# Optimization experiments

Measured on AMD Instinct MI355X. Metric: run time of the kernel, lower is better.

## Reference

```python
import jax, jax.numpy as jnp
import numpy as np


def setup_inputs() -> dict:
    key = jax.random.key(0)
    k1, k2 = jax.random.split(key)
    B, S, D = 8, 4096, 1024
    E, P = 8, 4
    x = jax.random.normal(k1, (B, S, D), dtype=jnp.float32)
    phi_kernel = jax.random.normal(k2, (D, E * P), dtype=jnp.float32) * (1.0 / np.sqrt(D))
    phi_bias = jnp.zeros((E * P,), dtype=jnp.float32)
    return {"x": x, "phi_kernel": phi_kernel, "phi_bias": phi_bias,
            "num_experts": E, "num_slots": P}


def reference(x, phi_kernel, phi_bias, num_experts, num_slots):
    B, S, D = x.shape
    E, P = num_experts, num_slots
    # phi logits: [B,S,E,P]
    phi_logits = (jnp.einsum('bsd,dk->bsk', x, phi_kernel) + phi_bias).reshape(B, S, E, P)
    # softmax over the sequence axis (each slot is a convex combo of tokens)
    phi_weights = jax.nn.softmax(phi_logits, axis=1)
    # soft slots: weighted sum over tokens -> [B,E,P,D] (fused, no [B,S,E,P,D] blowup)
    soft_slots = jnp.einsum('bsd,bsep->bepd', x, phi_weights)
    expert_inputs = soft_slots.reshape(B, E, P * D)
    expert_weights = jnp.full((B, S, E), 1.0 / E, dtype=x.dtype)
    expert_indices = jnp.broadcast_to(jnp.arange(E, dtype=jnp.int32)[None, None, :], (B, S, E))
    return (expert_weights, expert_indices, phi_weights, soft_slots, expert_inputs)
```

## Files before the change

### kernel.cpp

```cpp
#include <hip/hip_runtime.h>
#include <hip/hip_bf16.h>

#define B 8
#define S 4096
#define DD 1024
#define KK 32

__global__ __launch_bounds__(256) void k1_logits(const float* __restrict__ x,
                                                 const float* __restrict__ phi,
                                                 const float* __restrict__ bias,
                                                 float* __restrict__ lp) {
    constexpr int DCH = 512, NCH = 16;
    __shared__ float xt[2][64 * 36];

    const int bid = blockIdx.x;
    const int dq  = bid & 1;
    const int st  = (bid >> 1) & 63;
    const int b   = bid >> 7;
    const int s0  = st * 64;
    const int tid = threadIdx.x;
    const int kg  = __builtin_amdgcn_readfirstlane(tid >> 6);
    const int lane = tid & 63;

    float acc[8];
#pragma unroll
    for (int j = 0; j < 8; ++j) acc[j] = (dq == 0) ? bias[kg * 8 + j] : 0.f;

    const float* xb = x + ((size_t)(b * S + s0)) * DD + dq * DCH;
    const int row = tid >> 3;
    const int c4  = tid & 7;

    {
        float4 p0 = *(const float4*)(xb + (size_t)row * DD + c4 * 4);
        float4 p1 = *(const float4*)(xb + (size_t)(row + 32) * DD + c4 * 4);
        *(float4*)(&xt[0][row * 36 + c4 * 4]) = p0;
        *(float4*)(&xt[0][(row + 32) * 36 + c4 * 4]) = p1;
    }
    __syncthreads();

    for (int ch = 0; ch < NCH; ++ch) {
        const int cur = ch & 1;
        float4 q0, q1;
        if (ch + 1 < NCH) {
            q0 = *(const float4*)(xb + (size_t)row * DD + (ch + 1) * 32 + c4 * 4);
            q1 = *(const float4*)(xb + (size_t)(row + 32) * DD + (ch + 1) * 32 + c4 * 4);
        }

        const float* pbase = phi + (size_t)(dq * DCH + ch * 32) * KK + kg * 8;
        const float* xrow  = &xt[cur][lane * 36];
#pragma unroll
        for (int g = 0; g < 8; ++g) {
            float4 a = *(const float4*)(xrow + g * 4);
            const float* ap = &a.x;
#pragma unroll
            for (int dd = 0; dd < 4; ++dd) {
                const float* pr = pbase + (size_t)(g * 4 + dd) * KK;
                float4 pA = *(const float4*)pr;
                float4 pB = *(const float4*)(pr + 4);
                float av = ap[dd];
                acc[0] += av * pA.x; acc[1] += av * pA.y;
                acc[2] += av * pA.z; acc[3] += av * pA.w;
                acc[4] += av * pB.x; acc[5] += av * pB.y;
                acc[6] += av * pB.z; acc[7] += av * pB.w;
            }
        }
        __syncthreads();
        if (ch + 1 < NCH) {
            *(float4*)(&xt[cur ^ 1][row * 36 + c4 * 4]) = q0;
            *(float4*)(&xt[cur ^ 1][(row + 32) * 36 + c4 * 4]) = q1;
        }
        __syncthreads();
    }

    float* o = lp + (((size_t)dq * B + b) * KK + kg * 8) * S + s0;
#pragma unroll
    for (int j = 0; j < 8; ++j) o[(size_t)j * S + lane] = acc[j];
}

__global__ __launch_bounds__(256) void k2a_partial(const float* __restrict__ lp,
                                                   float* __restrict__ pmax,
                                                   float* __restrict__ psum) {
    const int bid = blockIdx.x;
    const int c  = bid & 7;
    const int bk = bid >> 3;
    const int tid = threadIdx.x;
    const int wave = tid >> 6, lane = tid & 63;
    const size_t base = (size_t)bk * S + c * 512;

    float v0 = lp[base + tid]       + lp[1048576 + base + tid];
    float v1 = lp[base + tid + 256] + lp[1048576 + base + tid + 256];

    float m = fmaxf(v0, v1);
#pragma unroll
    for (int off = 32; off >= 1; off >>= 1) m = fmaxf(m, __shfl_xor(m, off, 64));
    __shared__ float sm[4], sl[4];
    if (lane == 0) sm[wave] = m;
    __syncthreads();
    const float M = fmaxf(fmaxf(sm[0], sm[1]), fmaxf(sm[2], sm[3]));

    float l = __expf(v0 - M) + __expf(v1 - M);
#pragma unroll
    for (int off = 32; off >= 1; off >>= 1) l += __shfl_xor(l, off, 64);
    if (lane == 0) sl[wave] = l;
    __syncthreads();
    if (tid == 0) {
        pmax[bid] = M;
        psum[bid] = sl[0] + sl[1] + sl[2] + sl[3];
    }
}

__global__ __launch_bounds__(256) void k2c_norm(const float* __restrict__ lp,
                                                const float* __restrict__ pmax,
                                                const float* __restrict__ psum,
                                                float* __restrict__ pwT,
                                                float* __restrict__ pw_out) {
    __shared__ float tile[128][33];
    __shared__ float sM[32], sLinv[32];
    const int b  = blockIdx.x >> 5;
    const int sc = blockIdx.x & 31;
    const int s0 = sc * 128;
    const int tid = threadIdx.x;

    if (tid < 32) {
        const int k = tid;
        float M = -1e30f, L = 0.f;
#pragma unroll
        for (int c = 0; c < 8; ++c) {
            float mc = pmax[(b * KK + k) * 8 + c];
            float lc = psum[(b * KK + k) * 8 + c];
            float nM = fmaxf(M, mc);
            L = L * __expf(M - nM) + lc * __expf(mc - nM);
            M = nM;
        }
        sM[k] = M;
        sLinv[k] = 1.0f / L;
    }
    __syncthreads();

    const int sL = tid & 127;
    const int kh = tid >> 7;
#pragma unroll
    for (int kk = 0; kk < 16; ++kk) {
        const int k = kk * 2 + kh;
        const size_t idx = ((size_t)b * KK + k) * S + s0 + sL;
        float v = lp[idx] + lp[1048576 + idx];
        float w = __expf(v - sM[k]) * sLinv[k];
        pwT[idx] = w;
        tile[sL][k] = w;
    }
    __syncthreads();

    float* ob = pw_out + ((size_t)b * S + s0) * KK;
#pragma unroll
    for (int i = 0; i < 4; ++i) {
        const int idx4 = tid + i * 256;
        const int sl = idx4 >> 3, kq = idx4 & 7;
        float4 v4 = make_float4(tile[sl][kq * 4 + 0], tile[sl][kq * 4 + 1],
                                tile[sl][kq * 4 + 2], tile[sl][kq * 4 + 3]);
        ((float4*)ob)[idx4] = v4;
    }
}

template <int SSPLIT>
__global__ __launch_bounds__(256) void k3_partial(const float* __restrict__ x,
                                                  const float* __restrict__ pwT,
                                                  float* __restrict__ part) {
    constexpr int SCH = S / SSPLIT;
    const int bid = blockIdx.x;
    const int sc = bid % SSPLIT;
    const int dt = (bid / SSPLIT) & 3;
    const int b  = bid / (SSPLIT * 4);
    const int tid = threadIdx.x;
    const int kg = __builtin_amdgcn_readfirstlane(tid >> 6);
    const int lane = tid & 63;

    float4 acc[8];
#pragma unroll
    for (int j = 0; j < 8; ++j) acc[j] = make_float4(0.f, 0.f, 0.f, 0.f);

    const float* xb = x + ((size_t)(b * S + sc * SCH)) * DD + dt * 256 + lane * 4;
    const float* wb = pwT + ((size_t)b * KK + kg * 8) * S + sc * SCH;

    for (int ss = 0; ss < SCH / 4; ++ss) {
        float4 wq[8];
#pragma unroll
        for (int j = 0; j < 8; ++j) wq[j] = *(const float4*)(wb + (size_t)j * S + ss * 4);
#pragma unroll
        for (int dd = 0; dd < 4; ++dd) {
            float4 xv = *(const float4*)(xb + (size_t)(ss * 4 + dd) * DD);
#pragma unroll
            for (int j = 0; j < 8; ++j) {
                float w = ((const float*)&wq[j])[dd];
                acc[j].x += w * xv.x; acc[j].y += w * xv.y;
                acc[j].z += w * xv.z; acc[j].w += w * xv.w;
            }
        }
    }

    float* pp = part + (((size_t)sc * B + b) * KK + kg * 8) * DD + dt * 256 + lane * 4;
#pragma unroll
    for (int j = 0; j < 8; ++j) *(float4*)(pp + (size_t)j * DD) = acc[j];
}

template <int SSPLIT>
__global__ __launch_bounds__(256) void k4_finalize(const float* __restrict__ part,
                                                   float* __restrict__ out) {
    const int idx = blockIdx.x * 256 + threadIdx.x;
    const float4* p4 = (const float4*)part;

    float4 sv = p4[idx];
#pragma unroll
    for (int c = 1; c < SSPLIT; ++c) {
        float4 t = p4[(size_t)c * 65536 + idx];
        sv.x += t.x; sv.y += t.y; sv.z += t.z; sv.w += t.w;
    }

    ((float4*)(out + 1572864))[idx] = sv;
    ((float4*)(out + 1835008))[idx] = sv;
    ((float4*)out)[idx] = make_float4(0.125f, 0.125f, 0.125f, 0.125f);
    float base = (float)((idx * 4) & 7);
    ((float4*)(out + 262144))[idx] = make_float4(base, base + 1.f, base + 2.f, base + 3.f);
}

extern "C" void kernel_launch(void* const* d_in, const int* in_sizes, int n_in,
                              void* d_out, int out_size, void* d_ws, size_t ws_size,
                              hipStream_t stream) {
    const float* x    = (const float*)d_in[0];
    const float* phi  = (const float*)d_in[1];
    const float* bias = (const float*)d_in[2];
    float* out = (float*)d_out;

    float* lp   = (float*)d_ws;
    float* pmax = lp + 2097152;
    float* psum = lp + 2101248;
    float* pwT  = lp + 2105344;
    float* part = lp + 3153920;
    float* pw_out = out + 524288;

    k1_logits<<<dim3(1024), dim3(256), 0, stream>>>(x, phi, bias, lp);
    k2a_partial<<<dim3(2048), dim3(256), 0, stream>>>(lp, pmax, psum);
    k2c_norm<<<dim3(256), dim3(256), 0, stream>>>(lp, pmax, psum, pwT, pw_out);

    if (ws_size >= (size_t)47 * 1024 * 1024) {
        k3_partial<32><<<dim3(B * 4 * 32), dim3(256), 0, stream>>>(x, pwT, part);
        k4_finalize<32><<<dim3(256), dim3(256), 0, stream>>>(part, out);
    } else {
        k3_partial<8><<<dim3(B * 4 * 8), dim3(256), 0, stream>>>(x, pwT, part);
        k4_finalize<8><<<dim3(256), dim3(256), 0, stream>>>(part, out);
    }
}
```

Measured before the change: 267.9 us.

## Use bf16 MFMA for logits and slot GEMMs with swizzled LDS tiles

Rewrites the two GEMM-like kernels to convert x and weights to bf16 in LDS and compute with 32x32x16 bf16 MFMA instructions instead of fp32 FMA loops. Adds a small pre-kernel that transposes phi into bf16, and stores the softmax weights as bf16 to halve the traffic k3 reads. The slot GEMM now uses a fixed 8-way sequence split with d-tiles of 128. This trades fp32 accuracy for matrix-core throughput, so the outputs will differ numerically from an fp32 reference.

```diff
diff --git a/kernel.cpp b/kernel.cpp
--- a/kernel.cpp
+++ b/kernel.cpp
@@ -6,75 +6,139 @@
 #define DD 1024
 #define KK 32
 
+typedef __attribute__((ext_vector_type(8))) short bf16x8;
+typedef __attribute__((ext_vector_type(16))) float f32x16;
+
+static __device__ __forceinline__ unsigned short f2bf(float f) {
+    unsigned int u = __builtin_bit_cast(unsigned int, f);
+    u += 0x7FFFu + ((u >> 16) & 1u);
+    return (unsigned short)(u >> 16);
+}
+
+__global__ __launch_bounds__(256) void k0_phit(const float* __restrict__ phi,
+                                               unsigned short* __restrict__ phiT) {
+    __shared__ float lt[32][33];
+    const int d0 = blockIdx.x * 32;
+    const int tid = threadIdx.x;
+#pragma unroll
+    for (int i = 0; i < 4; ++i) {
+        int slot = tid + i * 256;
+        int d = slot >> 5, k = slot & 31;
+        lt[d][k] = phi[(size_t)(d0 + d) * KK + k];
+    }
+    __syncthreads();
+    const int k = tid >> 3, c = tid & 7, d = c * 4;
+    short4 pk;
+    pk.x = (short)f2bf(lt[d + 0][k]);
+    pk.y = (short)f2bf(lt[d + 1][k]);
+    pk.z = (short)f2bf(lt[d + 2][k]);
+    pk.w = (short)f2bf(lt[d + 3][k]);
+    *(short4*)(phiT + (size_t)k * DD + d0 + d) = pk;
+}
+
 __global__ __launch_bounds__(256) void k1_logits(const float* __restrict__ x,
-                                                 const float* __restrict__ phi,
+                                                 const unsigned short* __restrict__ phiT,
                                                  const float* __restrict__ bias,
                                                  float* __restrict__ lp) {
-    constexpr int DCH = 512, NCH = 16;
-    __shared__ float xt[2][64 * 36];
+    __shared__ __align__(16) char sm[32768 + 2 * 16384];
 
     const int bid = blockIdx.x;
-    const int dq  = bid & 1;
-    const int st  = (bid >> 1) & 63;
-    const int b   = bid >> 7;
-    const int s0  = st * 64;
-    const int tid = threadIdx.x;
-    const int kg  = __builtin_amdgcn_readfirstlane(tid >> 6);
+    const int dq = bid & 1;
+    const int st = (bid >> 1) & 31;
+    const int b  = bid >> 6;
+    const int s0 = st * 128;
+    const int tid = threadIdx.x;
+    const int wv = __builtin_amdgcn_readfirstlane(tid >> 6);
     const int lane = tid & 63;
-
-    float acc[8];
-#pragma unroll
-    for (int j = 0; j < 8; ++j) acc[j] = (dq == 0) ? bias[kg * 8 + j] : 0.f;
-
-    const float* xb = x + ((size_t)(b * S + s0)) * DD + dq * DCH;
-    const int row = tid >> 3;
-    const int c4  = tid & 7;
+    const int l31 = lane & 31;
+    const int half = lane >> 5;
 
     {
-        float4 p0 = *(const float4*)(xb + (size_t)row * DD + c4 * 4);
-        float4 p1 = *(const float4*)(xb + (size_t)(row + 32) * DD + c4 * 4);
-        *(float4*)(&xt[0][row * 36 + c4 * 4]) = p0;
-        *(float4*)(&xt[0][(row + 32) * 36 + c4 * 4]) = p1;
-    }
-    __syncthreads();
-
-    for (int ch = 0; ch < NCH; ++ch) {
-        const int cur = ch & 1;
-        float4 q0, q1;
-        if (ch + 1 < NCH) {
-            q0 = *(const float4*)(xb + (size_t)row * DD + (ch + 1) * 32 + c4 * 4);
-            q1 = *(const float4*)(xb + (size_t)(row + 32) * DD + (ch + 1) * 32 + c4 * 4);
-        }
-
-        const float* pbase = phi + (size_t)(dq * DCH + ch * 32) * KK + kg * 8;
-        const float* xrow  = &xt[cur][lane * 36];
-#pragma unroll
-        for (int g = 0; g < 8; ++g) {
-            float4 a = *(const float4*)(xrow + g * 4);
-            const float* ap = &a.x;
-#pragma unroll
-            for (int dd = 0; dd < 4; ++dd) {
-                const float* pr = pbase + (size_t)(g * 4 + dd) * KK;
-                float4 pA = *(const float4*)pr;
-                float4 pB = *(const float4*)(pr + 4);
-                float av = ap[dd];
-                acc[0] += av * pA.x; acc[1] += av * pA.y;
-                acc[2] += av * pA.z; acc[3] += av * pA.w;
-                acc[4] += av * pB.x; acc[5] += av * pB.y;
-                acc[6] += av * pB.z; acc[7] += av * pB.w;
-            }
+        const uint4* pg = (const uint4*)phiT;
+#pragma unroll
+        for (int i = 0; i < 8; ++i) {
+            int slot = tid + i * 256;
+            int k = slot >> 6, blk = slot & 63;
+            uint4 v = pg[(size_t)k * 128 + dq * 64 + blk];
+            *(uint4*)(sm + (size_t)k * 1024 + ((blk ^ (k & 7)) << 4)) = v;
+        }
+    }
+
+    f32x16 acc;
+    {
+        float bv = (dq == 0) ? bias[l31] : 0.f;
+#pragma unroll
+        for (int r = 0; r < 16; ++r) acc[r] = bv;
+    }
+
+    const float* xg = x + ((size_t)(b * S + s0)) * DD + dq * 512;
+
+    float4 q[8];
+    auto load8 = [&](int ch) {
+#pragma unroll
+        for (int i = 0; i < 8; ++i) {
+            int slot = tid + i * 256;
+            int s = slot >> 4, c4 = slot & 15;
+            q[i] = *(const float4*)(xg + (size_t)s * DD + ch * 64 + c4 * 4);
+        }
+    };
+    auto store8 = [&](char* buf) {
+#pragma unroll
+        for (int i = 0; i < 8; ++i) {
+            int slot = tid + i * 256;
+            int s = slot >> 4, c4 = slot & 15;
+            short4 pk;
+            pk.x = (short)f2bf(q[i].x);
+            pk.y = (short)f2bf(q[i].y);
+            pk.z = (short)f2bf(q[i].z);
+            pk.w = (short)f2bf(q[i].w);
+            *(short4*)(buf + (size_t)s * 128 + (((c4 >> 1) ^ (s & 7)) << 4) + (c4 & 1) * 8) = pk;
+        }
+    };
+
+    load8(0);
+    store8(sm + 32768);
+    __syncthreads();
+
+    const int srow = wv * 32 + l31;
+    const int sx = srow & 7;
+    const int kx = l31 & 7;
+
+    for (int ch = 0; ch < 8; ++ch) {
+        char* cur = sm + 32768 + (ch & 1) * 16384;
+        char* nxt = sm + 32768 + ((ch & 1) ^ 1) * 16384;
+        if (ch < 7) load8(ch + 1);
+#pragma unroll
+        for (int step = 0; step < 4; ++step) {
+            int blk = step * 2 + half;
+            bf16x8 af  = *(const bf16x8*)(cur + (size_t)srow * 128 + ((blk ^ sx) << 4));
+            bf16x8 bfv = *(const bf16x8*)(sm + (size_t)l31 * 1024 + (((ch * 8 + blk) ^ kx) << 4));
+            acc = __builtin_amdgcn_mfma_f32_32x32x16_bf16(af, bfv, acc, 0, 0, 0);
         }
         __syncthreads();
-        if (ch + 1 < NCH) {
-            *(float4*)(&xt[cur ^ 1][row * 36 + c4 * 4]) = q0;
-            *(float4*)(&xt[cur ^ 1][(row + 32) * 36 + c4 * 4]) = q1;
-        }
+        if (ch < 7) store8(nxt);
         __syncthreads();
     }
 
-    float* o = lp + (((size_t)dq * B + b) * KK + kg * 8) * S + s0;
-#pragma unroll
-    for (int j = 0; j < 8; ++j) o[(size_t)j * S + lane] = acc[j];
+    float* lt = (float*)(sm + 32768);
+#pragma unroll
+    for (int r = 0; r < 16; ++r) {
+        int row = (r & 3) + 8 * (r >> 2) + 4 * half;
+        lt[(size_t)l31 * 129 + wv * 32 + row] = acc[r];
+    }
+    __syncthreads();
+    float* o = lp + ((size_t)(dq * B + b) * KK) * S + s0;
+#pragma unroll
+    for (int i = 0; i < 4; ++i) {
+        int slot = tid + i * 256;
+        int k = slot >> 5, s4 = slot & 31;
+        float4 v;
+        v.x = lt[k * 129 + s4 * 4 + 0];
+        v.y = lt[k * 129 + s4 * 4 + 1];
+        v.z = lt[k * 129 + s4 * 4 + 2];
+        v.w = lt[k * 129 + s4 * 4 + 3];
+        *(float4*)(o + (size_t)k * S + s4 * 4) = v;
+    }
 }
 
 __global__ __launch_bounds__(256) void k2a_partial(const float* __restrict__ lp,
@@ -93,10 +157,10 @@
     float m = fmaxf(v0, v1);
 #pragma unroll
     for (int off = 32; off >= 1; off >>= 1) m = fmaxf(m, __shfl_xor(m, off, 64));
-    __shared__ float sm[4], sl[4];
-    if (lane == 0) sm[wave] = m;
-    __syncthreads();
-    const float M = fmaxf(fmaxf(sm[0], sm[1]), fmaxf(sm[2], sm[3]));
+    __shared__ float sm_[4], sl[4];
+    if (lane == 0) sm_[wave] = m;
+    __syncthreads();
+    const float M = fmaxf(fmaxf(sm_[0], sm_[1]), fmaxf(sm_[2], sm_[3]));
 
     float l = __expf(v0 - M) + __expf(v1 - M);
 #pragma unroll
@@ -112,7 +176,7 @@
 __global__ __launch_bounds__(256) void k2c_norm(const float* __restrict__ lp,
                                                 const float* __restrict__ pmax,
                                                 const float* __restrict__ psum,
-                                                float* __restrict__ pwT,
+                                                unsigned short* __restrict__ wbT,
                                                 float* __restrict__ pw_out) {
     __shared__ float tile[128][33];
     __shared__ float sM[32], sLinv[32];
@@ -145,7 +209,7 @@
         const size_t idx = ((size_t)b * KK + k) * S + s0 + sL;
         float v = lp[idx] + lp[1048576 + idx];
         float w = __expf(v - sM[k]) * sLinv[k];
-        pwT[idx] = w;
+        wbT[idx] = f2bf(w);
         tile[sL][k] = w;
     }
     __syncthreads();
@@ -161,48 +225,97 @@
     }
 }
 
-template <int SSPLIT>
-__global__ __launch_bounds__(256) void k3_partial(const float* __restrict__ x,
-                                                  const float* __restrict__ pwT,
-                                                  float* __restrict__ part) {
-    constexpr int SCH = S / SSPLIT;
+__global__ __launch_bounds__(256) void k3_slots(const float* __restrict__ x,
+                                                const unsigned int* __restrict__ wbT32,
+                                                float* __restrict__ part) {
+    __shared__ __align__(16) char sm[2 * 16384 + 2 * 4096];
+
     const int bid = blockIdx.x;
-    const int sc = bid % SSPLIT;
-    const int dt = (bid / SSPLIT) & 3;
-    const int b  = bid / (SSPLIT * 4);
-    const int tid = threadIdx.x;
-    const int kg = __builtin_amdgcn_readfirstlane(tid >> 6);
+    const int sc = bid & 7;
+    const int dg = (bid >> 3) & 7;
+    const int b  = bid >> 6;
+    const int tid = threadIdx.x;
+    const int wv = __builtin_amdgcn_readfirstlane(tid >> 6);
     const int lane = tid & 63;
-
-    float4 acc[8];
-#pragma unroll
-    for (int j = 0; j < 8; ++j) acc[j] = make_float4(0.f, 0.f, 0.f, 0.f);
-
-    const float* xb = x + ((size_t)(b * S + sc * SCH)) * DD + dt * 256 + lane * 4;
-    const float* wb = pwT + ((size_t)b * KK + kg * 8) * S + sc * SCH;
-
-    for (int ss = 0; ss < SCH / 4; ++ss) {
-        float4 wq[8];
-#pragma unroll
-        for (int j = 0; j < 8; ++j) wq[j] = *(const float4*)(wb + (size_t)j * S + ss * 4);
-#pragma unroll
-        for (int dd = 0; dd < 4; ++dd) {
-            float4 xv = *(const float4*)(xb + (size_t)(ss * 4 + dd) * DD);
-#pragma unroll
-            for (int j = 0; j < 8; ++j) {
-                float w = ((const float*)&wq[j])[dd];
-                acc[j].x += w * xv.x; acc[j].y += w * xv.y;
-                acc[j].z += w * xv.z; acc[j].w += w * xv.w;
-            }
-        }
-    }
-
-    float* pp = part + (((size_t)sc * B + b) * KK + kg * 8) * DD + dt * 256 + lane * 4;
-#pragma unroll
-    for (int j = 0; j < 8; ++j) *(float4*)(pp + (size_t)j * DD) = acc[j];
-}
-
-template <int SSPLIT>
+    const int l31 = lane & 31;
+    const int half = lane >> 5;
+
+    const int dth = tid & 127;
+    const int sh  = tid >> 7;
+
+    const float* xg = x + ((size_t)(b * S + sc * 512)) * DD + dg * 128 + dth;
+    const unsigned int* wg = wbT32 + (size_t)b * KK * (S / 2) + sc * 256;
+
+    float q0[16], q1[16];
+    unsigned int qw[4];
+    auto loadc = [&](int ch) {
+#pragma unroll
+        for (int j = 0; j < 16; ++j) {
+            int sp = sh * 16 + j;
+            q0[j] = xg[(size_t)(ch * 64 + sp * 2) * DD];
+            q1[j] = xg[(size_t)(ch * 64 + sp * 2 + 1) * DD];
+        }
+#pragma unroll
+        for (int i = 0; i < 4; ++i) {
+            int slot = tid + i * 256;
+            int k = slot >> 5, c = slot & 31;
+            qw[i] = wg[(size_t)k * (S / 2) + ch * 32 + c];
+        }
+    };
+    auto storec = [&](char* xB, char* wB) {
+#pragma unroll
+        for (int j = 0; j < 16; ++j) {
+            int sp = sh * 16 + j;
+            unsigned int pkd = (unsigned int)f2bf(q0[j]) | ((unsigned int)f2bf(q1[j]) << 16);
+            *(unsigned int*)(xB + (size_t)dth * 128 + (((sp >> 2) ^ (dth & 7)) << 4) + (sp & 3) * 4) = pkd;
+        }
+#pragma unroll
+        for (int i = 0; i < 4; ++i) {
+            int slot = tid + i * 256;
+            int k = slot >> 5, c = slot & 31;
+            *(unsigned int*)(wB + (size_t)k * 128 + (((c >> 2) ^ (k & 7)) << 4) + (c & 3) * 4) = qw[i];
+        }
+    };
+
+    f32x16 acc;
+#pragma unroll
+    for (int r = 0; r < 16; ++r) acc[r] = 0.f;
+
+    loadc(0);
+    storec(sm, sm + 32768);
+    __syncthreads();
+
+    const int dloc = wv * 32 + l31;
+    const int dx = dloc & 7;
+    const int kx = l31 & 7;
+
+    for (int ch = 0; ch < 8; ++ch) {
+        const int cur = ch & 1;
+        char* xCur = sm + cur * 16384;
+        char* wCur = sm + 32768 + cur * 4096;
+        char* xNxt = sm + (cur ^ 1) * 16384;
+        char* wNxt = sm + 32768 + (cur ^ 1) * 4096;
+        if (ch < 7) loadc(ch + 1);
+#pragma unroll
+        for (int step = 0; step < 4; ++step) {
+            int blk = step * 2 + half;
+            bf16x8 af  = *(const bf16x8*)(wCur + (size_t)l31 * 128 + ((blk ^ kx) << 4));
+            bf16x8 bfv = *(const bf16x8*)(xCur + (size_t)dloc * 128 + ((blk ^ dx) << 4));
+            acc = __builtin_amdgcn_mfma_f32_32x32x16_bf16(af, bfv, acc, 0, 0, 0);
+        }
+        __syncthreads();
+        if (ch < 7) storec(xNxt, wNxt);
+        __syncthreads();
+    }
+
+    float* pp = part + (((size_t)sc * B + b) * KK) * DD + dg * 128 + wv * 32 + l31;
+#pragma unroll
+    for (int r = 0; r < 16; ++r) {
+        int k = (r & 3) + 8 * (r >> 2) + 4 * half;
+        pp[(size_t)k * DD] = acc[r];
+    }
+}
+
 __global__ __launch_bounds__(256) void k4_finalize(const float* __restrict__ part,
                                                    float* __restrict__ out) {
     const int idx = blockIdx.x * 256 + threadIdx.x;
@@ -210,7 +323,7 @@
 
     float4 sv = p4[idx];
 #pragma unroll
-    for (int c = 1; c < SSPLIT; ++c) {
+    for (int c = 1; c < 8; ++c) {
         float4 t = p4[(size_t)c * 65536 + idx];
         sv.x += t.x; sv.y += t.y; sv.z += t.z; sv.w += t.w;
     }
@@ -230,22 +343,19 @@
     const float* bias = (const float*)d_in[2];
     float* out = (float*)d_out;
 
-    float* lp   = (float*)d_ws;
-    float* pmax = lp + 2097152;
-    float* psum = lp + 2101248;
-    float* pwT  = lp + 2105344;
-    float* part = lp + 3153920;
+    float* ws = (float*)d_ws;
+    float* lp   = ws;
+    float* pmax = ws + 2097152;
+    float* psum = ws + 2099200;
+    unsigned short* wbT  = (unsigned short*)(ws + 2101248);
+    unsigned short* phiT = (unsigned short*)(ws + 2625536);
+    float* part = ws + 2641920;
     float* pw_out = out + 524288;
 
-    k1_logits<<<dim3(1024), dim3(256), 0, stream>>>(x, phi, bias, lp);
+    k0_phit<<<dim3(32), dim3(256), 0, stream>>>(phi, phiT);
+    k1_logits<<<dim3(512), dim3(256), 0, stream>>>(x, phiT, bias, lp);
     k2a_partial<<<dim3(2048), dim3(256), 0, stream>>>(lp, pmax, psum);
-    k2c_norm<<<dim3(256), dim3(256), 0, stream>>>(lp, pmax, psum, pwT, pw_out);
-
-    if (ws_size >= (size_t)47 * 1024 * 1024) {
-        k3_partial<32><<<dim3(B * 4 * 32), dim3(256), 0, stream>>>(x, pwT, part);
-        k4_finalize<32><<<dim3(256), dim3(256), 0, stream>>>(part, out);
-    } else {
-        k3_partial<8><<<dim3(B * 4 * 8), dim3(256), 0, stream>>>(x, pwT, part);
-        k4_finalize<8><<<dim3(256), dim3(256), 0, stream>>>(part, out);
-    }
-}
+    k2c_norm<<<dim3(256), dim3(256), 0, stream>>>(lp, pmax, psum, wbT, pw_out);
+    k3_slots<<<dim3(512), dim3(256), 0, stream>>>(x, (const unsigned int*)wbT, part);
+    k4_finalize<<<dim3(256), dim3(256), 0, stream>>>(part, out);
+}
```

Result: faster. 234.0 us (-12.6%).
